# Kernel optimization log

Measured on AMD Instinct MI355X. Metric: run time of the kernel, lower is better.

## Reference

```python
import jax, jax.numpy as jnp
import numpy as np

B, T, HID = 1, 2048, 1024
H, D, S, KMAX = 16, 64, 64, 8


def local_attention(q, k, v, W):
    # lucidrains LocalAttention: causal, look_backward=1, autopad, scale=D**-0.5
    b, h, t, d = q.shape
    pad = (-t) % W
    qp = jnp.pad(q, ((0, 0), (0, 0), (0, pad), (0, 0)))
    kp = jnp.pad(k, ((0, 0), (0, 0), (0, pad), (0, 0)))
    vp = jnp.pad(v, ((0, 0), (0, 0), (0, pad), (0, 0)))
    tp = t + pad
    nw = tp // W
    qw = qp.reshape(b, h, nw, W, d)
    kw = kp.reshape(b, h, nw, W, d)
    vw = vp.reshape(b, h, nw, W, d)

    def look_back(x):  # prepend previous window (zeros for window 0)
        prev = jnp.pad(x, ((0, 0), (0, 0), (1, 0), (0, 0), (0, 0)))[:, :, :nw]
        return jnp.concatenate([prev, x], axis=3)  # (b,h,nw,2W,d)

    kk, vv = look_back(kw), look_back(vw)
    pos = jnp.arange(tp).reshape(nw, W)
    kpos = jnp.concatenate(
        [jnp.pad(pos, ((1, 0), (0, 0)), constant_values=-1)[:nw], pos], axis=1)  # (nw,2W)
    scores = jnp.einsum('bhnwd,bhnkd->bhnwk', qw, kk) * (d ** -0.5)
    valid = (pos[:, :, None] >= kpos[:, None, :]) & (kpos[:, None, :] >= 0)
    scores = jnp.where(valid[None, None], scores, -jnp.finfo(scores.dtype).max)
    probs = jax.nn.softmax(scores, axis=-1)
    out = jnp.einsum('bhnwk,bhnkd->bhnwd', probs, vv).reshape(b, h, tp, d)
    return out[:, :, :t]


def setup_inputs() -> dict:
    key = jax.random.key(0)
    ks = jax.random.split(key, 9)
    sd = 0.02
    return {
        'hidden_states': jax.random.normal(ks[0], (B, T, HID), jnp.float32),
        'Wq': jax.random.normal(ks[1], (HID, H * D), jnp.float32) * sd,
        'Wk': jax.random.normal(ks[2], (HID, H * D), jnp.float32) * sd,
        'Wv': jax.random.normal(ks[3], (HID, H * D), jnp.float32) * sd,
        'Wo': jax.random.normal(ks[4], (H * D, HID), jnp.float32) * sd,
        'Wc': jax.random.normal(ks[5], (S * D, D), jnp.float32) * sd,
        'bc': jax.random.normal(ks[6], (D,), jnp.float32) * sd,
        'k_scale': jnp.ones((1, H, 1), jnp.float32),
        'k_bias': jnp.zeros((1, H, 1), jnp.float32),
        'Wg': jax.random.normal(ks[7], (HID, 3 * H), jnp.float32) * sd,
        'bg': jax.random.normal(ks[8], (3 * H,), jnp.float32) * sd,
    }


def reference(hidden_states, Wq, Wk, Wv, Wo, Wc, bc, k_scale, k_bias, Wg, bg):
    b, t, _ = hidden_states.shape
    scale = D ** -0.5
    q = (hidden_states @ Wq).reshape(b, t, H, D).transpose(0, 2, 1, 3)
    k = (hidden_states @ Wk).reshape(b, t, H, D).transpose(0, 2, 1, 3)
    v = (hidden_states @ Wv).reshape(b, t, H, D).transpose(0, 2, 1, 3)

    sw_out = local_attention(q, k, v, S)

    pad = (-t) % S
    qp = jnp.pad(q, ((0, 0), (0, 0), (0, pad), (0, 0)))
    kp = jnp.pad(k, ((0, 0), (0, 0), (0, pad), (0, 0)))
    vp = jnp.pad(v, ((0, 0), (0, 0), (0, pad), (0, 0)))
    tp = t + pad
    nb = tp // S

    # compressed branch: shared compress MLP for k and v (same weights in torch)
    k_blk = kp.reshape(b, H, nb, S * D)
    v_blk = vp.reshape(b, H, nb, S * D)
    kc = jax.nn.gelu(k_blk @ Wc + bc, approximate=False)  # (b,H,nb,D)
    vc = jax.nn.gelu(v_blk @ Wc + bc, approximate=False)

    importance = jnp.einsum('bhid,bhjd->bhij', qp, kc) * scale  # (b,H,tp,nb)
    comp_probs = jax.nn.softmax(importance, axis=-1)
    comp_out = jnp.einsum('bhij,bhjd->bhid', comp_probs, vc)[:, :, :t]

    # block scores, entropy-driven dynamic top-k
    block_scores = importance.reshape(b, H, nb, S, nb).mean(axis=3)  # (b,H,nb,nb)
    block_probs = jax.nn.softmax(block_scores, axis=-1)
    entropy = -jnp.sum(block_probs * jnp.log(block_probs + 1e-9), axis=-1)
    max_entropy = jnp.log(jnp.float32(nb))
    norm_entropy = entropy / (max_entropy + 1e-9)  # (b,H,nb)
    k_logit = k_scale * norm_entropy + k_bias
    k_ratio = jax.nn.sigmoid(k_logit)
    dynamic_k = jnp.clip(KMAX * k_ratio, 1, KMAX).astype(jnp.int32)
    avg_k = dynamic_k.astype(jnp.float32).mean()

    _, topk_idx = jax.lax.top_k(block_scores, KMAX)  # (b,H,nb,KMAX)
    k_mask = jnp.arange(KMAX)[None, None, None, :] < dynamic_k[..., None]
    sel = (topk_idx[..., None] == jnp.arange(nb)) & k_mask[..., None]  # (b,H,nb,K,nb)
    mask = sel.any(axis=-2) | jnp.eye(nb, dtype=bool)  # (b,H,nb,nb)
    sparse_mask = jnp.repeat(jnp.repeat(mask, S, axis=2), S, axis=3)  # (b,H,tp,tp)

    attn = jnp.einsum('bhid,bhjd->bhij', qp, kp) * scale
    attn = jnp.where(sparse_mask, attn, -jnp.finfo(attn.dtype).max)
    fine_probs = jax.nn.softmax(attn, axis=-1)
    fine_out = jnp.einsum('bhij,bhjd->bhid', fine_probs, vp)[:, :, :t]

    gate = jax.nn.sigmoid(hidden_states @ Wg + bg)  # (b,t,3H)
    gate = gate.reshape(b, t, H, 3).transpose(0, 2, 1, 3)  # (b,H,t,3)
    combined = jnp.stack([sw_out, comp_out, fine_out], axis=-1)  # (b,H,t,D,3)
    out = jnp.einsum('bhnds,bhns->bhnd', combined, gate)
    merged = out.transpose(0, 2, 1, 3).reshape(b, t, H * D)
    output = merged @ Wo
    return output, avg_k, k_ratio, norm_entropy
```

## Files before the change

kernel.cpp:

```cpp
#include <hip/hip_runtime.h>
#include <math.h>

#define TT 2048
#define NH 16
#define HD 64
#define NB 32
#define HIDDEN 1024

typedef short s8v __attribute__((ext_vector_type(8)));
typedef float f4v __attribute__((ext_vector_type(4)));

__device__ __forceinline__ unsigned short f2bf(float x){
  unsigned u = __float_as_uint(x);
  unsigned r = (u + 0x7fffu + ((u>>16)&1u)) >> 16;
  return (unsigned short)r;
}
__device__ __forceinline__ float bf2f(unsigned short b){
  return __uint_as_float(((unsigned)b)<<16);
}
__device__ __forceinline__ void bsplit(float x, unsigned short& h, unsigned short& l){
  h = f2bf(x);
  l = f2bf(x - bf2f(h));
}

__device__ __forceinline__ float rmax32(float v){
#pragma unroll
  for(int o=16;o>0;o>>=1) v = fmaxf(v, __shfl_xor(v,o,32));
  return v;
}
__device__ __forceinline__ float rsum32(float v){
#pragma unroll
  for(int o=16;o>0;o>>=1) v += __shfl_xor(v,o,32);
  return v;
}

__global__ __launch_bounds__(256) void prep_all(
    const float* __restrict__ hs,
    const float* __restrict__ Wq, const float* __restrict__ Wk,
    const float* __restrict__ Wv, const float* __restrict__ Wo,
    const float* __restrict__ Wc,
    unsigned short* __restrict__ hh, unsigned short* __restrict__ hl,
    unsigned short* __restrict__ wth, unsigned short* __restrict__ wtl,
    unsigned short* __restrict__ woth,
    unsigned short* __restrict__ wcth, unsigned short* __restrict__ wctl)
{
  __shared__ float L[64][68];
  int bx = blockIdx.x;
  int t = threadIdx.x;
  if(bx < 2048){
    int i = (bx*256 + t)*4;
    float4 x = *(const float4*)(hs + i);
    ushort4 hv, lv;
    bsplit(x.x, hv.x, lv.x); bsplit(x.y, hv.y, lv.y);
    bsplit(x.z, hv.z, lv.z); bsplit(x.w, hv.w, lv.w);
    *(ushort4*)(hh + i) = hv;
    *(ushort4*)(hl + i) = lv;
    return;
  }
  if(bx < 3072){
    int idx = bx - 2048;
    int z = idx>>8, ky = (idx>>4)&15, nx = idx&15;
    const float* W = (z==0)?Wq:((z==1)?Wk:((z==2)?Wv:Wo));
    int k0 = ky*64, n0 = nx*64;
    int rr = t>>2, cg = t&3;
    const float* src = W + (size_t)(k0+rr)*1024 + n0 + cg*16;
    float4 a = *(const float4*)(src);
    float4 b = *(const float4*)(src+4);
    float4 c = *(const float4*)(src+8);
    float4 d = *(const float4*)(src+12);
    *(float4*)&L[rr][cg*16+0]  = a;
    *(float4*)&L[rr][cg*16+4]  = b;
    *(float4*)&L[rr][cg*16+8]  = c;
    *(float4*)&L[rr][cg*16+12] = d;
    __syncthreads();
    int nr = t>>2, kg = t&3;
    unsigned short hb[16], lb[16];
#pragma unroll
    for(int j=0;j<16;j++){
      float v = L[kg*16+j][nr];
      bsplit(v, hb[j], lb[j]);
    }
    if(z<3){
      size_t orow = ((size_t)z*1024 + n0 + nr)*1024 + k0 + kg*16;
      *(ushort4*)(wth+orow+0)  = make_ushort4(hb[0],hb[1],hb[2],hb[3]);
      *(ushort4*)(wth+orow+4)  = make_ushort4(hb[4],hb[5],hb[6],hb[7]);
      *(ushort4*)(wth+orow+8)  = make_ushort4(hb[8],hb[9],hb[10],hb[11]);
      *(ushort4*)(wth+orow+12) = make_ushort4(hb[12],hb[13],hb[14],hb[15]);
      *(ushort4*)(wtl+orow+0)  = make_ushort4(lb[0],lb[1],lb[2],lb[3]);
      *(ushort4*)(wtl+orow+4)  = make_ushort4(lb[4],lb[5],lb[6],lb[7]);
      *(ushort4*)(wtl+orow+8)  = make_ushort4(lb[8],lb[9],lb[10],lb[11]);
      *(ushort4*)(wtl+orow+12) = make_ushort4(lb[12],lb[13],lb[14],lb[15]);
    }else{
      size_t orow = ((size_t)n0 + nr)*1024 + k0 + kg*16;
      *(ushort4*)(woth+orow+0)  = make_ushort4(hb[0],hb[1],hb[2],hb[3]);
      *(ushort4*)(woth+orow+4)  = make_ushort4(hb[4],hb[5],hb[6],hb[7]);
      *(ushort4*)(woth+orow+8)  = make_ushort4(hb[8],hb[9],hb[10],hb[11]);
      *(ushort4*)(woth+orow+12) = make_ushort4(hb[12],hb[13],hb[14],hb[15]);
    }
    return;
  }
  {
    int k0 = (bx - 3072)*64;
    int rr = t>>2, cg = t&3;
    const float* src = Wc + (size_t)(k0+rr)*64 + cg*16;
    float4 a = *(const float4*)(src);
    float4 b = *(const float4*)(src+4);
    float4 c = *(const float4*)(src+8);
    float4 d = *(const float4*)(src+12);
    *(float4*)&L[rr][cg*16+0]  = a;
    *(float4*)&L[rr][cg*16+4]  = b;
    *(float4*)&L[rr][cg*16+8]  = c;
    *(float4*)&L[rr][cg*16+12] = d;
    __syncthreads();
    int nr = t>>2, kg = t&3;
    unsigned short hb[16], lb[16];
#pragma unroll
    for(int j=0;j<16;j++){
      float v = L[kg*16+j][nr];
      bsplit(v, hb[j], lb[j]);
    }
    size_t orow = (size_t)nr*4096 + k0 + kg*16;
    *(ushort4*)(wcth+orow+0)  = make_ushort4(hb[0],hb[1],hb[2],hb[3]);
    *(ushort4*)(wcth+orow+4)  = make_ushort4(hb[4],hb[5],hb[6],hb[7]);
    *(ushort4*)(wcth+orow+8)  = make_ushort4(hb[8],hb[9],hb[10],hb[11]);
    *(ushort4*)(wcth+orow+12) = make_ushort4(hb[12],hb[13],hb[14],hb[15]);
    *(ushort4*)(wctl+orow+0)  = make_ushort4(lb[0],lb[1],lb[2],lb[3]);
    *(ushort4*)(wctl+orow+4)  = make_ushort4(lb[4],lb[5],lb[6],lb[7]);
    *(ushort4*)(wctl+orow+8)  = make_ushort4(lb[8],lb[9],lb[10],lb[11]);
    *(ushort4*)(wctl+orow+12) = make_ushort4(lb[12],lb[13],lb[14],lb[15]);
  }
}

#define LROW 40
__global__ __launch_bounds__(256) void mfma_qkv_k(
    const unsigned short* __restrict__ ahg, const unsigned short* __restrict__ alg,
    const unsigned short* __restrict__ bhg, const unsigned short* __restrict__ blg,
    unsigned short* __restrict__ qbh, unsigned short* __restrict__ qbl,
    unsigned short* __restrict__ kbh, unsigned short* __restrict__ kbl,
    unsigned short* __restrict__ vbh)
{
  __shared__ unsigned short Ah[128*LROW], Al[128*LROW], Bh[128*LROW], Bl[128*LROW];
  int tid = threadIdx.x;
  int bn = blockIdx.x*128, bm = blockIdx.y*128;
  bool tp = (blockIdx.x < 16);
  int sr = tid>>2, skg = tid&3;
  const unsigned short* gA  = ahg + (size_t)(bm+sr)*HIDDEN + skg*8;
  const unsigned short* gAl = alg + (size_t)(bm+sr)*HIDDEN + skg*8;
  const unsigned short* gB  = bhg + (size_t)(bn+sr)*HIDDEN + skg*8;
  const unsigned short* gBl = blg + (size_t)(bn+sr)*HIDDEN + skg*8;
  int wv = tid>>6, ln = tid&63;
  int wm = (wv&1)*64, wn = (wv>>1)*64;
  int fr = ln&15, fq = ln>>4;
  int wlds = sr*LROW + skg*8;
  f4v acc[4][4] = {};
  for(int k0=0;k0<HIDDEN;k0+=32){
    s8v a0 = *(const s8v*)(gA + k0);
    s8v a1 = *(const s8v*)(gA + 65536 + k0);
    s8v b0 = *(const s8v*)(gB + k0);
    s8v b1 = *(const s8v*)(gB + 65536 + k0);
    s8v a0l, a1l, b0l, b1l;
    if(tp){
      a0l = *(const s8v*)(gAl + k0);
      a1l = *(const s8v*)(gAl + 65536 + k0);
      b0l = *(const s8v*)(gBl + k0);
      b1l = *(const s8v*)(gBl + 65536 + k0);
    }
    __syncthreads();
    *(s8v*)&Ah[wlds] = a0; *(s8v*)&Ah[wlds + 64*LROW] = a1;
    *(s8v*)&Bh[wlds] = b0; *(s8v*)&Bh[wlds + 64*LROW] = b1;
    if(tp){
      *(s8v*)&Al[wlds] = a0l; *(s8v*)&Al[wlds + 64*LROW] = a1l;
      *(s8v*)&Bl[wlds] = b0l; *(s8v*)&Bl[wlds + 64*LROW] = b1l;
    }
    __syncthreads();
    s8v af[4], bf[4], tf;
#pragma unroll
    for(int i=0;i<4;i++) af[i] = *(const s8v*)&Ah[(wm+i*16+fr)*LROW + fq*8];
#pragma unroll
    for(int i=0;i<4;i++) bf[i] = *(const s8v*)&Bh[(wn+i*16+fr)*LROW + fq*8];
#pragma unroll
    for(int i=0;i<4;i++)
#pragma unroll
      for(int j=0;j<4;j++)
        acc[i][j] = __builtin_amdgcn_mfma_f32_16x16x32_bf16(af[i], bf[j], acc[i][j], 0,0,0);
    if(tp){
#pragma unroll
      for(int i=0;i<4;i++){
        tf = *(const s8v*)&Al[(wm+i*16+fr)*LROW + fq*8];
#pragma unroll
        for(int j=0;j<4;j++)
          acc[i][j] = __builtin_amdgcn_mfma_f32_16x16x32_bf16(tf, bf[j], acc[i][j], 0,0,0);
      }
#pragma unroll
      for(int j=0;j<4;j++){
        tf = *(const s8v*)&Bl[(wn+j*16+fr)*LROW + fq*8];
#pragma unroll
        for(int i=0;i<4;i++)
          acc[i][j] = __builtin_amdgcn_mfma_f32_16x16x32_bf16(af[i], tf, acc[i][j], 0,0,0);
      }
    }
  }
  int z = bn >> 10;
#pragma unroll
  for(int i=0;i<4;i++){
    int mb = bm + wm + i*16 + fq*4;
#pragma unroll
    for(int j=0;j<4;j++){
      int n = bn + wn + j*16 + fr;
      int n1 = n & 1023, hd = n1>>6, d = n1&63;
      size_t base = ((size_t)hd*TT + mb)*HD + d;
#pragma unroll
      for(int r=0;r<4;r++){
        float v = acc[i][j][r];
        size_t a = base + (size_t)r*HD;
        if(z==0){
          unsigned short hi = f2bf(v);
          qbh[a] = hi; qbl[a] = f2bf(v - bf2f(hi));
        }else if(z==1){
          unsigned short hi = f2bf(v);
          kbh[a] = hi; kbl[a] = f2bf(v - bf2f(hi));
        }else{
          vbh[a] = f2bf(v);
        }
      }
    }
  }
}

__global__ __launch_bounds__(256) void conv_vt(
    const unsigned short* __restrict__ vbh, unsigned short* __restrict__ vth)
{
  int tt = blockIdx.x, h = blockIdx.y;
  __shared__ unsigned short L[64][72];
  int t = threadIdx.x;
  int row = t>>2, dg = (t&3)*16;
  const unsigned short* src = vbh + ((size_t)h*TT + tt*64 + row)*HD + dg;
  *(s8v*)&L[row][dg]   = *(const s8v*)(src);
  *(s8v*)&L[row][dg+8] = *(const s8v*)(src+8);
  __syncthreads();
  int d = t>>2, kg = (t&3)*16;
  s8v r0, r1;
#pragma unroll
  for(int u=0;u<8;u++)  r0[u] = (short)L[kg+u][d];
#pragma unroll
  for(int u=0;u<8;u++)  r1[u] = (short)L[kg+8+u][d];
  unsigned short* dst = vth + ((size_t)h*HD + d)*TT + tt*64 + kg;
  *(s8v*)(dst)   = r0;
  *(s8v*)(dst+8) = r1;
}

__global__ __launch_bounds__(256) void gate_kernel(
    const float* __restrict__ hs, const float* __restrict__ Wg, const float* __restrict__ bg,
    float* __restrict__ gatep)
{
  int t = blockIdx.x;
  __shared__ float row[1024];
  __shared__ float red[4][64];
  int tid = threadIdx.x;
  *(float4*)(row + tid*4) = *(const float4*)(hs + (size_t)t*HIDDEN + tid*4);
  __syncthreads();
  int n = tid & 63, part = tid>>6;
  float s = 0.f;
  if(n < 48){
    const float* w = Wg + n;
    for(int kx = part*256; kx < part*256+256; kx++)
      s += row[kx]*w[(size_t)kx*48];
  }
  red[part][n] = s;
  __syncthreads();
  if(part==0 && n<48){
    float x = red[0][n]+red[1][n]+red[2][n]+red[3][n] + bg[n];
    gatep[(size_t)t*48 + n] = 1.f/(1.f+expf(-x));
  }
}

#define CROW 40
__global__ __launch_bounds__(256) void mfma_compress_k(
    const unsigned short* __restrict__ kbh, const unsigned short* __restrict__ kbl,
    const unsigned short* __restrict__ vbh,
    const unsigned short* __restrict__ wcth, const unsigned short* __restrict__ wctl,
    float* __restrict__ ccpart)
{
  __shared__ unsigned short As[64*CROW], Al[64*CROW], Bs[64*CROW], Bl[64*CROW];
  int chunk = blockIdx.x;
  int mt = blockIdx.y;
  bool isK = (mt < 8);
  const unsigned short* Ag  = isK ? (kbh + (size_t)mt*262144) : (vbh + (size_t)(mt-8)*262144);
  const unsigned short* Agl = kbl + (size_t)(isK ? mt : 0)*262144;
  int tid = threadIdx.x;
  int sr = tid>>2, skg = (tid&3)*8;
  int k0b = chunk*512;
  const unsigned short* gA  = Ag  + (size_t)sr*4096 + k0b + skg;
  const unsigned short* gAl = Agl + (size_t)sr*4096 + k0b + skg;
  const unsigned short* gB  = wcth + (size_t)sr*4096 + k0b + skg;
  const unsigned short* gBl = wctl + (size_t)sr*4096 + k0b + skg;
  int wv = tid>>6, ln = tid&63;
  int fr = ln&15, fq = ln>>4;
  int wlds = sr*CROW + skg;
  f4v acc[4] = {};
  for(int ks=0; ks<512; ks+=32){
    s8v a0 = *(const s8v*)(gA + ks);
    s8v b0 = *(const s8v*)(gB + ks);
    s8v b1 = *(const s8v*)(gBl + ks);
    s8v a1 = {};
    if(isK) a1 = *(const s8v*)(gAl + ks);
    __syncthreads();
    *(s8v*)&As[wlds] = a0;
    *(s8v*)&Bs[wlds] = b0;
    *(s8v*)&Bl[wlds] = b1;
    if(isK) *(s8v*)&Al[wlds] = a1;
    __syncthreads();
    s8v bfh = *(const s8v*)&Bs[(wv*16+fr)*CROW + fq*8];
    s8v bfl = *(const s8v*)&Bl[(wv*16+fr)*CROW + fq*8];
#pragma unroll
    for(int m=0;m<4;m++){
      s8v af = *(const s8v*)&As[(m*16+fr)*CROW + fq*8];
      acc[m] = __builtin_amdgcn_mfma_f32_16x16x32_bf16(af, bfh, acc[m], 0,0,0);
      acc[m] = __builtin_amdgcn_mfma_f32_16x16x32_bf16(af, bfl, acc[m], 0,0,0);
      if(isK){
        s8v afl = *(const s8v*)&Al[(m*16+fr)*CROW + fq*8];
        acc[m] = __builtin_amdgcn_mfma_f32_16x16x32_bf16(afl, bfh, acc[m], 0,0,0);
      }
    }
  }
  float* dst = ccpart + ((size_t)chunk*1024 + mt*64)*64;
#pragma unroll
  for(int m=0;m<4;m++)
#pragma unroll
    for(int r=0;r<4;r++)
      dst[(size_t)(m*16+fq*4+r)*64 + wv*16 + fr] = acc[m][r];
}

__global__ __launch_bounds__(256) void compress_fin(
    const float* __restrict__ ccpart, const float* __restrict__ bcp,
    unsigned short* __restrict__ kch, unsigned short* __restrict__ kcl,
    unsigned short* __restrict__ vcth)
{
  int idx = blockIdx.x*256 + threadIdx.x;
  int row = idx>>6, col = idx&63;
  float s = 0.f;
#pragma unroll
  for(int c=0;c<8;c++) s += ccpart[(size_t)c*65536 + idx];
  s += bcp[col];
  float g = 0.5f*s*(1.f+erff(s*0.70710678118654752f));
  if(row < 512){
    unsigned short hi = f2bf(g);
    kch[idx] = hi;
    kcl[idx] = f2bf(g - bf2f(hi));
  }else{
    int r = row - 512;
    int h = r>>5, j = r&31;
    vcth[((size_t)h*64 + col)*32 + j] = f2bf(g);
  }
}

__global__ __launch_bounds__(256) void comp_attn_mfma(
    const unsigned short* __restrict__ qbh, const unsigned short* __restrict__ qbl,
    const unsigned short* __restrict__ kch, const unsigned short* __restrict__ kcl,
    const unsigned short* __restrict__ vcth,
    float* __restrict__ imp, float* __restrict__ comp)
{
  __shared__ unsigned short Pl[4*16*40];
  int tid = threadIdx.x;
  int wave = __builtin_amdgcn_readfirstlane(tid>>6);
  int ln = tid&63;
  int fr = ln&15, fq = ln>>4;
  int i = blockIdx.x, h = blockIdx.y;

  const unsigned short* qrh = qbh + ((size_t)h*TT + i*64 + wave*16 + fr)*HD + fq*8;
  const unsigned short* qrl = qbl + ((size_t)h*TT + i*64 + wave*16 + fr)*HD + fq*8;
  s8v bh0 = *(const s8v*)(qrh);
  s8v bh1 = *(const s8v*)(qrh + 32);
  s8v bl0 = *(const s8v*)(qrl);
  s8v bl1 = *(const s8v*)(qrl + 32);

  f4v sv[2] = {};
#pragma unroll
  for(int mt=0;mt<2;mt++){
    const unsigned short* ar = kch + ((size_t)h*32 + mt*16 + fr)*HD + fq*8;
    const unsigned short* al = kcl + ((size_t)h*32 + mt*16 + fr)*HD + fq*8;
    s8v ah0 = *(const s8v*)(ar);
    s8v ah1 = *(const s8v*)(ar + 32);
    s8v al0 = *(const s8v*)(al);
    s8v al1 = *(const s8v*)(al + 32);
    sv[mt] = __builtin_amdgcn_mfma_f32_16x16x32_bf16(ah0, bh0, sv[mt], 0,0,0);
    sv[mt] = __builtin_amdgcn_mfma_f32_16x16x32_bf16(ah1, bh1, sv[mt], 0,0,0);
    sv[mt] = __builtin_amdgcn_mfma_f32_16x16x32_bf16(al0, bh0, sv[mt], 0,0,0);
    sv[mt] = __builtin_amdgcn_mfma_f32_16x16x32_bf16(al1, bh1, sv[mt], 0,0,0);
    sv[mt] = __builtin_amdgcn_mfma_f32_16x16x32_bf16(ah0, bl0, sv[mt], 0,0,0);
    sv[mt] = __builtin_amdgcn_mfma_f32_16x16x32_bf16(ah1, bl1, sv[mt], 0,0,0);
  }
  int t = i*64 + wave*16 + fr;
  float* impr = imp + ((size_t)h*TT + t)*NB;
  float mx = -3.4e38f;
#pragma unroll
  for(int mt=0;mt<2;mt++)
#pragma unroll
    for(int r=0;r<4;r++){
      float s = sv[mt][r]*0.125f;
      sv[mt][r] = s;
      impr[mt*16 + fq*4 + r] = s;
      mx = fmaxf(mx, s);
    }
  mx = fmaxf(mx, __shfl_xor(mx,16,64));
  mx = fmaxf(mx, __shfl_xor(mx,32,64));
  unsigned short* Pw = Pl + wave*16*40;
  float es = 0.f;
#pragma unroll
  for(int mt=0;mt<2;mt++)
#pragma unroll
    for(int r=0;r<4;r++){
      float p = __expf(sv[mt][r] - mx);
      es += p;
      Pw[fr*40 + mt*16 + fq*4 + r] = f2bf(p);
    }
  es += __shfl_xor(es,16,64);
  es += __shfl_xor(es,32,64);

  s8v ap = *(const s8v*)&Pw[fr*40 + fq*8];
  f4v acc[4] = {};
#pragma unroll
  for(int nt=0;nt<4;nt++){
    s8v bv = *(const s8v*)(vcth + ((size_t)h*64 + nt*16 + fr)*32 + fq*8);
    acc[nt] = __builtin_amdgcn_mfma_f32_16x16x32_bf16(ap, bv, acc[nt], 0,0,0);
  }
  float lv[4];
#pragma unroll
  for(int r=0;r<4;r++) lv[r] = __shfl(es, fq*4+r, 64);
#pragma unroll
  for(int nt=0;nt<4;nt++)
#pragma unroll
    for(int r=0;r<4;r++){
      int tq = i*64 + wave*16 + fq*4 + r;
      comp[((size_t)h*TT + tq)*HD + nt*16 + fr] = acc[nt][r]/lv[r];
    }
}

__global__ __launch_bounds__(256) void block_stats(
    const float* __restrict__ imp, const float* __restrict__ ksc, const float* __restrict__ kbi,
    unsigned* __restrict__ maskb, float* __restrict__ dkf,
    float* __restrict__ out_kratio, float* __restrict__ out_nent)
{
  int hb = blockIdx.x; int h = hb>>5, i = hb&31;
  int tid = threadIdx.x; int j = tid&31, p = tid>>5;
  const float* base = imp + ((size_t)h*TT + i*64)*NB;
  float s = 0.f;
  for(int t2=p*8; t2<p*8+8; t2++) s += base[(size_t)t2*NB + j];
  __shared__ float red[8][32];
  red[p][j] = s;
  __syncthreads();
  if(tid < 32){
    float bs = 0.f;
#pragma unroll
    for(int pp=0; pp<8; pp++) bs += red[pp][j];
    bs *= (1.f/64.f);
    float m = rmax32(bs);
    float e = expf(bs - m);
    float se = rsum32(e);
    float prob = e/se;
    float ent = rsum32(-prob * logf(prob + 1e-9f));
    float nent = ent / (3.4657359027997265f + 1e-9f);
    float kl = ksc[h]*nent + kbi[h];
    float kr = 1.f/(1.f + expf(-kl));
    float dkfl = fminf(fmaxf(8.f*kr, 1.f), 8.f);
    int dk = (int)dkfl;
    unsigned sel = 0u;
    for(int r=0;r<dk;r++){
      bool unpicked = ((sel>>j)&1u)==0u;
      float cand = unpicked ? bs : -3.4e38f;
      float mx = rmax32(cand);
      unsigned long long b = __ballot(cand == mx);
      int idxsel = __ffsll(b & 0xffffffffull) - 1;
      sel |= (1u<<idxsel);
    }
    sel |= (1u<<i);
    if(j==0){
      maskb[hb] = sel;
      dkf[hb] = (float)dk;
      out_kratio[hb] = kr;
      out_nent[hb] = nent;
    }
  }
}

__global__ __launch_bounds__(256) void avgk_kernel(const float* __restrict__ dkf, float* __restrict__ outp){
  __shared__ float red[256];
  int tid=threadIdx.x;
  red[tid] = dkf[tid] + dkf[tid+256];
  __syncthreads();
  for(int s=128;s>0;s>>=1){ if(tid<s) red[tid]+=red[tid+s]; __syncthreads(); }
  if(tid==0) outp[0] = red[0] * (1.f/512.f);
}

__global__ __launch_bounds__(256) void attn_fused(
    const unsigned short* __restrict__ qbh, const unsigned short* __restrict__ kbh,
    const unsigned short* __restrict__ vth, const unsigned* __restrict__ maskb,
    const float* __restrict__ comp, const float* __restrict__ gatep,
    unsigned short* __restrict__ mergedh)
{
  __shared__ unsigned short Kb[64*72];
  __shared__ unsigned short Vt[64*72];
  __shared__ unsigned short Pf[4*16*72];
  __shared__ unsigned short Ps[4*16*72];
  int tid = threadIdx.x;
  int wave = __builtin_amdgcn_readfirstlane(tid>>6);
  int ln = tid & 63;
  int fr = ln & 15, fq = ln >> 4;
  int hb = blockIdx.x; int h = hb>>5, i = hb&31;
  unsigned mb_s = (1u<<i) | (i ? (1u<<(i-1)) : 0u);
  unsigned mb_f = maskb[hb];
  unsigned mb = mb_s | mb_f;

  const unsigned short* qrow = qbh + ((size_t)h*TT + i*64 + wave*16 + fr)*HD + fq*8;
  s8v bq0 = *(const s8v*)(qrow);
  s8v bq1 = *(const s8v*)(qrow + 32);

  f4v acc_f[4] = {}, acc_s[4] = {};
  float mf = -3.4e38f, lf = 0.f, ms = -3.4e38f, ls = 0.f;

  int srow = tid>>2, sg = (tid&3)*16;
  unsigned short* Pfw = Pf + wave*16*72;
  unsigned short* Psw = Ps + wave*16*72;
  int qpos = wave*16 + fr;

  for(int j=0;j<NB;j++){
    if(!((mb>>j)&1u)) continue;
    __syncthreads();
    {
      const unsigned short* ks_ = kbh + ((size_t)h*TT + j*64 + srow)*HD + sg;
      *(s8v*)&Kb[srow*72 + sg]     = *(const s8v*)(ks_);
      *(s8v*)&Kb[srow*72 + sg + 8] = *(const s8v*)(ks_ + 8);
      const unsigned short* vs_ = vth + ((size_t)h*HD + srow)*TT + j*64 + sg;
      *(s8v*)&Vt[srow*72 + sg]     = *(const s8v*)(vs_);
      *(s8v*)&Vt[srow*72 + sg + 8] = *(const s8v*)(vs_ + 8);
    }
    __syncthreads();

    f4v sv[4] = {};
#pragma unroll
    for(int mt=0;mt<4;mt++){
      s8v ak0 = *(const s8v*)&Kb[(mt*16+fr)*72 + fq*8];
      s8v ak1 = *(const s8v*)&Kb[(mt*16+fr)*72 + fq*8 + 32];
      sv[mt] = __builtin_amdgcn_mfma_f32_16x16x32_bf16(ak0, bq0, sv[mt], 0,0,0);
      sv[mt] = __builtin_amdgcn_mfma_f32_16x16x32_bf16(ak1, bq1, sv[mt], 0,0,0);
    }
#pragma unroll
    for(int mt=0;mt<4;mt++)
#pragma unroll
      for(int r=0;r<4;r++) sv[mt][r] *= 0.125f;

    bool in_f = ((mb_f>>j)&1u) != 0u;
    bool in_s = (j==i) || (j+1==i);

    if(in_f){
      float mx = -3.4e38f;
#pragma unroll
      for(int mt=0;mt<4;mt++)
#pragma unroll
        for(int r=0;r<4;r++) mx = fmaxf(mx, sv[mt][r]);
      mx = fmaxf(mx, __shfl_xor(mx,16,64));
      mx = fmaxf(mx, __shfl_xor(mx,32,64));
      float mnew = fmaxf(mf, mx);
      float es = 0.f;
#pragma unroll
      for(int mt=0;mt<4;mt++)
#pragma unroll
        for(int r=0;r<4;r++){
          float p = __expf(sv[mt][r] - mnew);
          es += p;
          Pfw[fr*72 + mt*16 + fq*4 + r] = f2bf(p);
        }
      es += __shfl_xor(es,16,64);
      es += __shfl_xor(es,32,64);
      float alpha = __expf(mf - mnew);
      lf = lf*alpha + es;
      mf = mnew;
      float av[4];
#pragma unroll
      for(int r=0;r<4;r++) av[r] = __shfl(alpha, fq*4+r, 64);
#pragma unroll
      for(int nt=0;nt<4;nt++)
#pragma unroll
        for(int r=0;r<4;r++) acc_f[nt][r] *= av[r];
    }
    if(in_s){
      if(j==i){
#pragma unroll
        for(int mt=0;mt<4;mt++)
#pragma unroll
          for(int r=0;r<4;r++)
            if((mt*16 + fq*4 + r) > qpos) sv[mt][r] = -3.4e38f;
      }
      float mx = -3.4e38f;
#pragma unroll
      for(int mt=0;mt<4;mt++)
#pragma unroll
        for(int r=0;r<4;r++) mx = fmaxf(mx, sv[mt][r]);
      mx = fmaxf(mx, __shfl_xor(mx,16,64));
      mx = fmaxf(mx, __shfl_xor(mx,32,64));
      float mnew = fmaxf(ms, mx);
      float es = 0.f;
#pragma unroll
      for(int mt=0;mt<4;mt++)
#pragma unroll
        for(int r=0;r<4;r++){
          float p = __expf(sv[mt][r] - mnew);
          es += p;
          Psw[fr*72 + mt*16 + fq*4 + r] = f2bf(p);
        }
      es += __shfl_xor(es,16,64);
      es += __shfl_xor(es,32,64);
      float alpha = __expf(ms - mnew);
      ls = ls*alpha + es;
      ms = mnew;
      float av[4];
#pragma unroll
      for(int r=0;r<4;r++) av[r] = __shfl(alpha, fq*4+r, 64);
#pragma unroll
      for(int nt=0;nt<4;nt++)
#pragma unroll
        for(int r=0;r<4;r++) acc_s[nt][r] *= av[r];
    }

    if(in_f){
      s8v ap0 = *(const s8v*)&Pfw[fr*72 + fq*8];
      s8v ap1 = *(const s8v*)&Pfw[fr*72 + fq*8 + 32];
#pragma unroll
      for(int nt=0;nt<4;nt++){
        s8v bv0 = *(const s8v*)&Vt[(nt*16+fr)*72 + fq*8];
        s8v bv1 = *(const s8v*)&Vt[(nt*16+fr)*72 + fq*8 + 32];
        acc_f[nt] = __builtin_amdgcn_mfma_f32_16x16x32_bf16(ap0, bv0, acc_f[nt], 0,0,0);
        acc_f[nt] = __builtin_amdgcn_mfma_f32_16x16x32_bf16(ap1, bv1, acc_f[nt], 0,0,0);
      }
    }
    if(in_s){
      s8v ap0 = *(const s8v*)&Psw[fr*72 + fq*8];
      s8v ap1 = *(const s8v*)&Psw[fr*72 + fq*8 + 32];
#pragma unroll
      for(int nt=0;nt<4;nt++){
        s8v bv0 = *(const s8v*)&Vt[(nt*16+fr)*72 + fq*8];
        s8v bv1 = *(const s8v*)&Vt[(nt*16+fr)*72 + fq*8 + 32];
        acc_s[nt] = __builtin_amdgcn_mfma_f32_16x16x32_bf16(ap0, bv0, acc_s[nt], 0,0,0);
        acc_s[nt] = __builtin_amdgcn_mfma_f32_16x16x32_bf16(ap1, bv1, acc_s[nt], 0,0,0);
      }
    }
  }

  float lvf[4], lvs[4], g0[4], g1[4], g2[4];
#pragma unroll
  for(int r=0;r<4;r++){
    lvf[r] = __shfl(lf, fq*4+r, 64);
    lvs[r] = __shfl(ls, fq*4+r, 64);
    int t = i*64 + wave*16 + fq*4 + r;
    const float* g = gatep + (size_t)t*48 + h*3;
    g0[r] = g[0]; g1[r] = g[1]; g2[r] = g[2];
  }
#pragma unroll
  for(int nt=0;nt<4;nt++){
#pragma unroll
    for(int r=0;r<4;r++){
      int t = i*64 + wave*16 + fq*4 + r;
      int d = nt*16 + fr;
      float of = acc_f[nt][r] / lvf[r];
      float os = acc_s[nt][r] / lvs[r];
      float cp = comp[((size_t)h*TT + t)*HD + d];
      mergedh[(size_t)t*1024 + h*64 + d] = f2bf(g0[r]*os + g1[r]*cp + g2[r]*of);
    }
  }
}

__global__ __launch_bounds__(256) void mfma_proj_k(
    const unsigned short* __restrict__ ahg, const unsigned short* __restrict__ bhg,
    float* __restrict__ C)
{
  __shared__ unsigned short Ah[128*LROW], Bh[128*LROW];
  int tid = threadIdx.x;
  int bn = blockIdx.x*128, bm = blockIdx.y*128;
  int sr = tid>>2, skg = tid&3;
  const unsigned short* gA = ahg + (size_t)(bm+sr)*HIDDEN + skg*8;
  const unsigned short* gB = bhg + (size_t)(bn+sr)*HIDDEN + skg*8;
  int wv = tid>>6, ln = tid&63;
  int wm = (wv&1)*64, wn = (wv>>1)*64;
  int fr = ln&15, fq = ln>>4;
  int wlds = sr*LROW + skg*8;
  f4v acc[4][4] = {};
  for(int k0=0;k0<HIDDEN;k0+=32){
    s8v a0 = *(const s8v*)(gA + k0);
    s8v a1 = *(const s8v*)(gA + 65536 + k0);
    s8v b0 = *(const s8v*)(gB + k0);
    s8v b1 = *(const s8v*)(gB + 65536 + k0);
    __syncthreads();
    *(s8v*)&Ah[wlds] = a0; *(s8v*)&Ah[wlds + 64*LROW] = a1;
    *(s8v*)&Bh[wlds] = b0; *(s8v*)&Bh[wlds + 64*LROW] = b1;
    __syncthreads();
    s8v af[4], bf[4];
#pragma unroll
    for(int i=0;i<4;i++) af[i] = *(const s8v*)&Ah[(wm+i*16+fr)*LROW + fq*8];
#pragma unroll
    for(int i=0;i<4;i++) bf[i] = *(const s8v*)&Bh[(wn+i*16+fr)*LROW + fq*8];
#pragma unroll
    for(int i=0;i<4;i++)
#pragma unroll
      for(int j=0;j<4;j++)
        acc[i][j] = __builtin_amdgcn_mfma_f32_16x16x32_bf16(af[i], bf[j], acc[i][j], 0,0,0);
  }
#pragma unroll
  for(int i=0;i<4;i++){
    int mb = bm + wm + i*16 + fq*4;
#pragma unroll
    for(int j=0;j<4;j++){
      int n = bn + wn + j*16 + fr;
      float* dst = C + (size_t)mb*HIDDEN + n;
#pragma unroll
      for(int r=0;r<4;r++) dst[(size_t)r*HIDDEN] = acc[i][j][r];
    }
  }
}

extern "C" void kernel_launch(void* const* d_in, const int* in_sizes, int n_in,
                              void* d_out, int out_size, void* d_ws, size_t ws_size,
                              hipStream_t stream) {
  (void)in_sizes; (void)n_in; (void)out_size; (void)ws_size;
  const float* hs  = (const float*)d_in[0];
  const float* Wq  = (const float*)d_in[1];
  const float* Wk  = (const float*)d_in[2];
  const float* Wv  = (const float*)d_in[3];
  const float* Wo  = (const float*)d_in[4];
  const float* Wc  = (const float*)d_in[5];
  const float* bcp = (const float*)d_in[6];
  const float* ksc = (const float*)d_in[7];
  const float* kbi = (const float*)d_in[8];
  const float* Wg  = (const float*)d_in[9];
  const float* bg  = (const float*)d_in[10];
  float* out = (float*)d_out;

  float* ws = (float*)d_ws;
  float* gatep  = ws;
  unsigned short* kch  = (unsigned short*)(gatep + 98304);
  unsigned short* kcl  = kch + 32768;
  unsigned short* vcth = kcl + 32768;
  float* imp    = gatep + 98304 + 65536;
  float* comp   = imp + 1048576;
  float* wthf   = comp + 2097152;
  float* wtlf   = wthf + 1572864;
  unsigned short* mergedh = (unsigned short*)(wtlf + 1572864);
  float* dkf    = wtlf + 1572864 + 1048576;
  unsigned* maskb = (unsigned*)(dkf + 512);
  unsigned short* woth = (unsigned short*)(dkf + 1024);
  unsigned short* qbh  = (unsigned short*)(dkf + 1024 + 524288);
  unsigned short* qbl  = qbh + 2097152;
  unsigned short* kbh  = qbl + 2097152;
  unsigned short* kbl  = kbh + 2097152;
  unsigned short* vbh  = kbl + 2097152;
  unsigned short* vth  = vbh + 2097152;
  unsigned short* wcth = vth + 2097152;
  unsigned short* wctl = wcth + 262144;
  float* ccpart = (float*)(wctl + 262144);

  unsigned short* hsh = (unsigned short*)comp;
  unsigned short* hsl = (unsigned short*)(comp + 1048576);
  unsigned short* wth = (unsigned short*)wthf;
  unsigned short* wtl = (unsigned short*)wtlf;

  float* out_avgk   = out + 2097152;
  float* out_kratio = out + 2097153;
  float* out_nent   = out + 2097665;

  prep_all<<<dim3(3136), 256, 0, stream>>>(hs, Wq, Wk, Wv, Wo, Wc,
                                           hsh, hsl, wth, wtl, woth, wcth, wctl);
  mfma_qkv_k<<<dim3(24,16), 256, 0, stream>>>(hsh, hsl, wth, wtl,
                                              qbh, qbl, kbh, kbl, vbh);
  conv_vt<<<dim3(32,16), 256, 0, stream>>>(vbh, vth);
  gate_kernel<<<dim3(2048), 256, 0, stream>>>(hs, Wg, bg, gatep);
  mfma_compress_k<<<dim3(8,16), 256, 0, stream>>>(kbh, kbl, vbh, wcth, wctl, ccpart);
  compress_fin<<<dim3(256), 256, 0, stream>>>(ccpart, bcp, kch, kcl, vcth);
  comp_attn_mfma<<<dim3(32,16), 256, 0, stream>>>(qbh, qbl, kch, kcl, vcth, imp, comp);
  block_stats<<<dim3(512), 256, 0, stream>>>(imp, ksc, kbi, maskb, dkf, out_kratio, out_nent);
  avgk_kernel<<<dim3(1), 256, 0, stream>>>(dkf, out_avgk);
  attn_fused<<<dim3(512), 256, 0, stream>>>(qbh, kbh, vth, maskb, comp, gatep, mergedh);
  mfma_proj_k<<<dim3(8,16), 256, 0, stream>>>(mergedh, woth, out);
}
```

Measured before the change: 236.5 us.

## Fold gate GEMV into prep kernel, halve GEMM N-tiles, stage QKV epilogue via LDS

The gate projection moves into extra blocks of prep_all, which removes one kernel launch. The QKV and output-projection GEMMs switch from 128x128 to 128x64 tiles, doubling the block count to raise occupancy and spread work across more CUs. The QKV epilogue now stages bf16 results in shared memory and writes them with coalesced 16-byte stores instead of scattered 2-byte stores. Smaller tiles reduce operand reuse per block and increase global traffic for the A matrix.

```diff
diff --git a/kernel.cpp b/kernel.cpp
--- a/kernel.cpp
+++ b/kernel.cpp
@@ -39,12 +39,14 @@
     const float* __restrict__ Wq, const float* __restrict__ Wk,
     const float* __restrict__ Wv, const float* __restrict__ Wo,
     const float* __restrict__ Wc,
+    const float* __restrict__ Wg, const float* __restrict__ bg,
     unsigned short* __restrict__ hh, unsigned short* __restrict__ hl,
     unsigned short* __restrict__ wth, unsigned short* __restrict__ wtl,
     unsigned short* __restrict__ woth,
-    unsigned short* __restrict__ wcth, unsigned short* __restrict__ wctl)
-{
-  __shared__ float L[64][68];
+    unsigned short* __restrict__ wcth, unsigned short* __restrict__ wctl,
+    float* __restrict__ gatep)
+{
+  __shared__ float SL[64*68];
   int bx = blockIdx.x;
   int t = threadIdx.x;
   if(bx < 2048){
@@ -58,6 +60,7 @@
     return;
   }
   if(bx < 3072){
+    float (*L)[68] = (float(*)[68])SL;
     int idx = bx - 2048;
     int z = idx>>8, ky = (idx>>4)&15, nx = idx&15;
     const float* W = (z==0)?Wq:((z==1)?Wk:((z==2)?Wv:Wo));
@@ -99,7 +102,8 @@
     }
     return;
   }
-  {
+  if(bx < 3136){
+    float (*L)[68] = (float(*)[68])SL;
     int k0 = (bx - 3072)*64;
     int rr = t>>2, cg = t&3;
     const float* src = Wc + (size_t)(k0+rr)*64 + cg*16;
@@ -128,6 +132,27 @@
     *(ushort4*)(wctl+orow+4)  = make_ushort4(lb[4],lb[5],lb[6],lb[7]);
     *(ushort4*)(wctl+orow+8)  = make_ushort4(lb[8],lb[9],lb[10],lb[11]);
     *(ushort4*)(wctl+orow+12) = make_ushort4(lb[12],lb[13],lb[14],lb[15]);
+    return;
+  }
+  {
+    float* row = SL;
+    float (*red)[64] = (float(*)[64])(SL + 1024);
+    int tr = bx - 3136;
+    *(float4*)(row + t*4) = *(const float4*)(hs + (size_t)tr*HIDDEN + t*4);
+    __syncthreads();
+    int n = t & 63, part = t>>6;
+    float s = 0.f;
+    if(n < 48){
+      const float* w = Wg + n;
+      for(int kx = part*256; kx < part*256+256; kx++)
+        s += row[kx]*w[(size_t)kx*48];
+    }
+    red[part][n] = s;
+    __syncthreads();
+    if(part==0 && n<48){
+      float x = red[0][n]+red[1][n]+red[2][n]+red[3][n] + bg[n];
+      gatep[(size_t)tr*48 + n] = 1.f/(1.f+expf(-x));
+    }
   }
 }
 
@@ -139,61 +164,65 @@
     unsigned short* __restrict__ kbh, unsigned short* __restrict__ kbl,
     unsigned short* __restrict__ vbh)
 {
-  __shared__ unsigned short Ah[128*LROW], Al[128*LROW], Bh[128*LROW], Bl[128*LROW];
+  __shared__ unsigned short SH[15360];
+  unsigned short* SA  = SH;
+  unsigned short* SAl = SH + 5120;
+  unsigned short* SB  = SH + 10240;
+  unsigned short* SBl = SH + 12800;
   int tid = threadIdx.x;
-  int bn = blockIdx.x*128, bm = blockIdx.y*128;
-  bool tp = (blockIdx.x < 16);
-  int sr = tid>>2, skg = tid&3;
-  const unsigned short* gA  = ahg + (size_t)(bm+sr)*HIDDEN + skg*8;
-  const unsigned short* gAl = alg + (size_t)(bm+sr)*HIDDEN + skg*8;
-  const unsigned short* gB  = bhg + (size_t)(bn+sr)*HIDDEN + skg*8;
-  const unsigned short* gBl = blg + (size_t)(bn+sr)*HIDDEN + skg*8;
+  int bn = blockIdx.x*64, bm = blockIdx.y*128;
+  bool tp = (blockIdx.x < 32);
+  int aRow = tid>>1, aOff = (tid&1)*16;
+  int bRow = tid>>2, bOff = (tid&3)*8;
+  const unsigned short* gA  = ahg + (size_t)(bm+aRow)*HIDDEN + aOff;
+  const unsigned short* gAl = alg + (size_t)(bm+aRow)*HIDDEN + aOff;
+  const unsigned short* gB  = bhg + (size_t)(bn+bRow)*HIDDEN + bOff;
+  const unsigned short* gBl = blg + (size_t)(bn+bRow)*HIDDEN + bOff;
+  int wlA = aRow*LROW + aOff;
+  int wlB = bRow*LROW + bOff;
   int wv = tid>>6, ln = tid&63;
-  int wm = (wv&1)*64, wn = (wv>>1)*64;
+  int wm = (wv&1)*64, wn = (wv>>1)*32;
   int fr = ln&15, fq = ln>>4;
-  int wlds = sr*LROW + skg*8;
-  f4v acc[4][4] = {};
+  f4v acc[4][2] = {};
   for(int k0=0;k0<HIDDEN;k0+=32){
     s8v a0 = *(const s8v*)(gA + k0);
-    s8v a1 = *(const s8v*)(gA + 65536 + k0);
+    s8v a1 = *(const s8v*)(gA + k0 + 8);
     s8v b0 = *(const s8v*)(gB + k0);
-    s8v b1 = *(const s8v*)(gB + 65536 + k0);
-    s8v a0l, a1l, b0l, b1l;
+    s8v a0l, a1l, b0l;
     if(tp){
       a0l = *(const s8v*)(gAl + k0);
-      a1l = *(const s8v*)(gAl + 65536 + k0);
+      a1l = *(const s8v*)(gAl + k0 + 8);
       b0l = *(const s8v*)(gBl + k0);
-      b1l = *(const s8v*)(gBl + 65536 + k0);
-    }
-    __syncthreads();
-    *(s8v*)&Ah[wlds] = a0; *(s8v*)&Ah[wlds + 64*LROW] = a1;
-    *(s8v*)&Bh[wlds] = b0; *(s8v*)&Bh[wlds + 64*LROW] = b1;
+    }
+    __syncthreads();
+    *(s8v*)&SA[wlA] = a0; *(s8v*)&SA[wlA+8] = a1;
+    *(s8v*)&SB[wlB] = b0;
     if(tp){
-      *(s8v*)&Al[wlds] = a0l; *(s8v*)&Al[wlds + 64*LROW] = a1l;
-      *(s8v*)&Bl[wlds] = b0l; *(s8v*)&Bl[wlds + 64*LROW] = b1l;
-    }
-    __syncthreads();
-    s8v af[4], bf[4], tf;
-#pragma unroll
-    for(int i=0;i<4;i++) af[i] = *(const s8v*)&Ah[(wm+i*16+fr)*LROW + fq*8];
-#pragma unroll
-    for(int i=0;i<4;i++) bf[i] = *(const s8v*)&Bh[(wn+i*16+fr)*LROW + fq*8];
+      *(s8v*)&SAl[wlA] = a0l; *(s8v*)&SAl[wlA+8] = a1l;
+      *(s8v*)&SBl[wlB] = b0l;
+    }
+    __syncthreads();
+    s8v af[4], bf[2], tf;
+#pragma unroll
+    for(int i=0;i<4;i++) af[i] = *(const s8v*)&SA[(wm+i*16+fr)*LROW + fq*8];
+#pragma unroll
+    for(int j=0;j<2;j++) bf[j] = *(const s8v*)&SB[(wn+j*16+fr)*LROW + fq*8];
 #pragma unroll
     for(int i=0;i<4;i++)
 #pragma unroll
-      for(int j=0;j<4;j++)
+      for(int j=0;j<2;j++)
         acc[i][j] = __builtin_amdgcn_mfma_f32_16x16x32_bf16(af[i], bf[j], acc[i][j], 0,0,0);
     if(tp){
 #pragma unroll
       for(int i=0;i<4;i++){
-        tf = *(const s8v*)&Al[(wm+i*16+fr)*LROW + fq*8];
-#pragma unroll
-        for(int j=0;j<4;j++)
+        tf = *(const s8v*)&SAl[(wm+i*16+fr)*LROW + fq*8];
+#pragma unroll
+        for(int j=0;j<2;j++)
           acc[i][j] = __builtin_amdgcn_mfma_f32_16x16x32_bf16(tf, bf[j], acc[i][j], 0,0,0);
       }
 #pragma unroll
-      for(int j=0;j<4;j++){
-        tf = *(const s8v*)&Bl[(wn+j*16+fr)*LROW + fq*8];
+      for(int j=0;j<2;j++){
+        tf = *(const s8v*)&SBl[(wn+j*16+fr)*LROW + fq*8];
 #pragma unroll
         for(int i=0;i<4;i++)
           acc[i][j] = __builtin_amdgcn_mfma_f32_16x16x32_bf16(af[i], tf, acc[i][j], 0,0,0);
@@ -201,28 +230,41 @@
     }
   }
   int z = bn >> 10;
-#pragma unroll
-  for(int i=0;i<4;i++){
-    int mb = bm + wm + i*16 + fq*4;
-#pragma unroll
-    for(int j=0;j<4;j++){
-      int n = bn + wn + j*16 + fr;
-      int n1 = n & 1023, hd = n1>>6, d = n1&63;
-      size_t base = ((size_t)hd*TT + mb)*HD + d;
-#pragma unroll
-      for(int r=0;r<4;r++){
-        float v = acc[i][j][r];
-        size_t a = base + (size_t)r*HD;
-        if(z==0){
-          unsigned short hi = f2bf(v);
-          qbh[a] = hi; qbl[a] = f2bf(v - bf2f(hi));
-        }else if(z==1){
-          unsigned short hi = f2bf(v);
-          kbh[a] = hi; kbl[a] = f2bf(v - bf2f(hi));
-        }else{
-          vbh[a] = f2bf(v);
+  int head = (bn & 1023) >> 6;
+  unsigned short* Cs = SH;
+  unsigned short* dsth = (z==0)?qbh:((z==1)?kbh:vbh);
+  size_t obase = ((size_t)head*TT + bm)*HD;
+  __syncthreads();
+#pragma unroll
+  for(int i=0;i<4;i++)
+#pragma unroll
+    for(int j=0;j<2;j++)
+#pragma unroll
+      for(int r=0;r<4;r++)
+        Cs[(wm+i*16+fq*4+r)*64 + wn+j*16+fr] = f2bf(acc[i][j][r]);
+  __syncthreads();
+#pragma unroll
+  for(int u=0;u<4;u++){
+    int c = u*256 + tid;
+    *(s8v*)(dsth + obase + c*8) = *(const s8v*)&Cs[c*8];
+  }
+  if(z<2){
+    unsigned short* dstl = (z==0)?qbl:kbl;
+    __syncthreads();
+#pragma unroll
+    for(int i=0;i<4;i++)
+#pragma unroll
+      for(int j=0;j<2;j++)
+#pragma unroll
+        for(int r=0;r<4;r++){
+          float v = acc[i][j][r];
+          Cs[(wm+i*16+fq*4+r)*64 + wn+j*16+fr] = f2bf(v - bf2f(f2bf(v)));
         }
-      }
+    __syncthreads();
+#pragma unroll
+    for(int u=0;u<4;u++){
+      int c = u*256 + tid;
+      *(s8v*)(dstl + obase + c*8) = *(const s8v*)&Cs[c*8];
     }
   }
 }
@@ -247,31 +289,6 @@
   unsigned short* dst = vth + ((size_t)h*HD + d)*TT + tt*64 + kg;
   *(s8v*)(dst)   = r0;
   *(s8v*)(dst+8) = r1;
-}
-
-__global__ __launch_bounds__(256) void gate_kernel(
-    const float* __restrict__ hs, const float* __restrict__ Wg, const float* __restrict__ bg,
-    float* __restrict__ gatep)
-{
-  int t = blockIdx.x;
-  __shared__ float row[1024];
-  __shared__ float red[4][64];
-  int tid = threadIdx.x;
-  *(float4*)(row + tid*4) = *(const float4*)(hs + (size_t)t*HIDDEN + tid*4);
-  __syncthreads();
-  int n = tid & 63, part = tid>>6;
-  float s = 0.f;
-  if(n < 48){
-    const float* w = Wg + n;
-    for(int kx = part*256; kx < part*256+256; kx++)
-      s += row[kx]*w[(size_t)kx*48];
-  }
-  red[part][n] = s;
-  __syncthreads();
-  if(part==0 && n<48){
-    float x = red[0][n]+red[1][n]+red[2][n]+red[3][n] + bg[n];
-    gatep[(size_t)t*48 + n] = 1.f/(1.f+expf(-x));
-  }
 }
 
 #define CROW 40
@@ -673,42 +690,43 @@
     const unsigned short* __restrict__ ahg, const unsigned short* __restrict__ bhg,
     float* __restrict__ C)
 {
-  __shared__ unsigned short Ah[128*LROW], Bh[128*LROW];
+  __shared__ unsigned short SA[128*LROW], SB[64*LROW];
   int tid = threadIdx.x;
-  int bn = blockIdx.x*128, bm = blockIdx.y*128;
-  int sr = tid>>2, skg = tid&3;
-  const unsigned short* gA = ahg + (size_t)(bm+sr)*HIDDEN + skg*8;
-  const unsigned short* gB = bhg + (size_t)(bn+sr)*HIDDEN + skg*8;
+  int bn = blockIdx.x*64, bm = blockIdx.y*128;
+  int aRow = tid>>1, aOff = (tid&1)*16;
+  int bRow = tid>>2, bOff = (tid&3)*8;
+  const unsigned short* gA = ahg + (size_t)(bm+aRow)*HIDDEN + aOff;
+  const unsigned short* gB = bhg + (size_t)(bn+bRow)*HIDDEN + bOff;
+  int wlA = aRow*LROW + aOff;
+  int wlB = bRow*LROW + bOff;
   int wv = tid>>6, ln = tid&63;
-  int wm = (wv&1)*64, wn = (wv>>1)*64;
+  int wm = (wv&1)*64, wn = (wv>>1)*32;
   int fr = ln&15, fq = ln>>4;
-  int wlds = sr*LROW + skg*8;
-  f4v acc[4][4] = {};
+  f4v acc[4][2] = {};
   for(int k0=0;k0<HIDDEN;k0+=32){
     s8v a0 = *(const s8v*)(gA + k0);
-    s8v a1 = *(const s8v*)(gA + 65536 + k0);
+    s8v a1 = *(const s8v*)(gA + k0 + 8);
     s8v b0 = *(const s8v*)(gB + k0);
-    s8v b1 = *(const s8v*)(gB + 65536 + k0);
-    __syncthreads();
-    *(s8v*)&Ah[wlds] = a0; *(s8v*)&Ah[wlds + 64*LROW] = a1;
-    *(s8v*)&Bh[wlds] = b0; *(s8v*)&Bh[wlds + 64*LROW] = b1;
-    __syncthreads();
-    s8v af[4], bf[4];
-#pragma unroll
-    for(int i=0;i<4;i++) af[i] = *(const s8v*)&Ah[(wm+i*16+fr)*LROW + fq*8];
-#pragma unroll
-    for(int i=0;i<4;i++) bf[i] = *(const s8v*)&Bh[(wn+i*16+fr)*LROW + fq*8];
+    __syncthreads();
+    *(s8v*)&SA[wlA] = a0; *(s8v*)&SA[wlA+8] = a1;
+    *(s8v*)&SB[wlB] = b0;
+    __syncthreads();
+    s8v af[4], bf[2];
+#pragma unroll
+    for(int i=0;i<4;i++) af[i] = *(const s8v*)&SA[(wm+i*16+fr)*LROW + fq*8];
+#pragma unroll
+    for(int j=0;j<2;j++) bf[j] = *(const s8v*)&SB[(wn+j*16+fr)*LROW + fq*8];
 #pragma unroll
     for(int i=0;i<4;i++)
 #pragma unroll
-      for(int j=0;j<4;j++)
+      for(int j=0;j<2;j++)
         acc[i][j] = __builtin_amdgcn_mfma_f32_16x16x32_bf16(af[i], bf[j], acc[i][j], 0,0,0);
   }
 #pragma unroll
   for(int i=0;i<4;i++){
     int mb = bm + wm + i*16 + fq*4;
 #pragma unroll
-    for(int j=0;j<4;j++){
+    for(int j=0;j<2;j++){
       int n = bn + wn + j*16 + fr;
       float* dst = C + (size_t)mb*HIDDEN + n;
 #pragma unroll
@@ -766,17 +784,16 @@
   float* out_kratio = out + 2097153;
   float* out_nent   = out + 2097665;
 
-  prep_all<<<dim3(3136), 256, 0, stream>>>(hs, Wq, Wk, Wv, Wo, Wc,
-                                           hsh, hsl, wth, wtl, woth, wcth, wctl);
-  mfma_qkv_k<<<dim3(24,16), 256, 0, stream>>>(hsh, hsl, wth, wtl,
+  prep_all<<<dim3(5184), 256, 0, stream>>>(hs, Wq, Wk, Wv, Wo, Wc, Wg, bg,
+                                           hsh, hsl, wth, wtl, woth, wcth, wctl, gatep);
+  mfma_qkv_k<<<dim3(48,16), 256, 0, stream>>>(hsh, hsl, wth, wtl,
                                               qbh, qbl, kbh, kbl, vbh);
   conv_vt<<<dim3(32,16), 256, 0, stream>>>(vbh, vth);
-  gate_kernel<<<dim3(2048), 256, 0, stream>>>(hs, Wg, bg, gatep);
   mfma_compress_k<<<dim3(8,16), 256, 0, stream>>>(kbh, kbl, vbh, wcth, wctl, ccpart);
   compress_fin<<<dim3(256), 256, 0, stream>>>(ccpart, bcp, kch, kcl, vcth);
   comp_attn_mfma<<<dim3(32,16), 256, 0, stream>>>(qbh, qbl, kch, kcl, vcth, imp, comp);
   block_stats<<<dim3(512), 256, 0, stream>>>(imp, ksc, kbi, maskb, dkf, out_kratio, out_nent);
   avgk_kernel<<<dim3(1), 256, 0, stream>>>(dkf, out_avgk);
   attn_fused<<<dim3(512), 256, 0, stream>>>(qbh, kbh, vth, maskb, comp, gatep, mergedh);
-  mfma_proj_k<<<dim3(8,16), 256, 0, stream>>>(mergedh, woth, out);
-}
+  mfma_proj_k<<<dim3(16,16), 256, 0, stream>>>(mergedh, woth, out);
+}
```

Result: faster. 223.7 us (-5.4%).
